# Kernel optimization log

Hardware: AMD Instinct MI355X
Metric: run time of the kernel (lower is better)

Reference implementation:

```python
import jax, jax.numpy as jnp
import numpy as np

BIG = 10000.0

def setup_inputs() -> dict:
    key = jax.random.key(0)
    k1, k2, k3 = jax.random.split(key, 3)
    B, S, D = 32, 4096, 512
    x = jax.random.normal(k1, (B, S, D), dtype=jnp.float32)
    mask = jax.random.randint(k2, (B, S), 0, 2).astype(bool)
    w_attn = jax.random.normal(k3, (D, 1), dtype=jnp.float32)
    return {"x": x, "mask": mask, "w_attn": w_attn}

def reference(x, mask, w_attn):
    # x: [B, S, D], mask: [B, S] bool, w_attn: [D, 1]
    mask_f = mask.astype(jnp.float32)[:, :, None]          # [B, S, 1]
    masked_x = x * mask_f
    seq_len = jnp.sum(mask_f, axis=1) + 1e-6               # [B, 1]
    mean_pool = jnp.sum(masked_x, axis=1) / seq_len        # [B, D]

    m3 = mask[:, :, None]
    max_pool = jnp.max(jnp.where(m3, x, -BIG), axis=1)     # [B, D]
    min_pool = jnp.min(jnp.where(m3, x, BIG), axis=1)      # [B, D]

    attn_scores = jnp.einsum('bsd,do->bso', x, w_attn)     # [B, S, 1]
    attn_scores = jnp.where(m3, attn_scores, -BIG)
    attn_w = jax.nn.softmax(attn_scores, axis=1)           # [B, S, 1]
    attn_pool = jnp.sum(x * attn_w, axis=1)                # [B, D]

    return jnp.concatenate([mean_pool, max_pool, min_pool, attn_pool], axis=-1)
```

## Files before the change

### kernel.cpp

```cpp
#include <hip/hip_runtime.h>
#include <math.h>

#define BIGV 10000.0f

constexpr int B = 32, S = 4096, D = 512;
constexpr int C = 16;
constexpr int L = S / C;
constexpr int T = 16;
constexpr int NT = L / T;
constexpr int BC = B * C;

__global__ __launch_bounds__(512, 4)
void pool_partial(const float* __restrict__ x, const int* __restrict__ mask,
                  const float* __restrict__ w, float* __restrict__ ws) {
  __shared__ float xt[T][D];
  __shared__ float w_s[D];
  __shared__ float sc[T];
  __shared__ float pv[T];
  __shared__ int   mk[T];

  const int tid = threadIdx.x;
  const int blk = blockIdx.x;
  const int b = blk / C, c = blk % C;
  const int s0 = c * L;

  w_s[tid] = w[tid];

  float m = -INFINITY, l = 0.f, cnt = 0.f;
  float o = 0.f, sm = 0.f, mx = -BIGV, mn = BIGV;

  const float4* gsrc = (const float4*)(x + ((size_t)b * S + s0) * D);
  const int* gm = mask + (size_t)b * S + s0;

  const int wave = tid >> 6, lane = tid & 63;

  for (int t = 0; t < NT; ++t) {
    __syncthreads();
    const float4* src = gsrc + (size_t)t * (T * D / 4);
    float4* dst = (float4*)&xt[0][0];
    #pragma unroll
    for (int i = 0; i < (T * D / 4) / 512; ++i)
      dst[tid + i * 512] = src[tid + i * 512];
    if (tid < T) mk[tid] = gm[t * T + tid];
    __syncthreads();

    #pragma unroll
    for (int rr = 0; rr < T / 8; ++rr) {
      const int r = wave * (T / 8) + rr;
      float dacc = 0.f;
      #pragma unroll
      for (int k = 0; k < D / 64; ++k)
        dacc = fmaf(xt[r][lane + 64 * k], w_s[lane + 64 * k], dacc);
      #pragma unroll
      for (int off = 32; off; off >>= 1)
        dacc += __shfl_xor(dacc, off, 64);
      if (lane == 0) sc[r] = mk[r] ? dacc : -BIGV;
    }
    __syncthreads();

    float Mt = -INFINITY;
    #pragma unroll
    for (int r = 0; r < T; ++r) Mt = fmaxf(Mt, sc[r]);
    const float m_new = fmaxf(m, Mt);
    const float alpha = __expf(m - m_new);
    o *= alpha; l *= alpha;
    m = m_new;
    if (tid < T) pv[tid] = __expf(sc[tid] - m_new);
    __syncthreads();

    #pragma unroll
    for (int r = 0; r < T; ++r) {
      const float p    = pv[r];
      const int   mb   = mk[r];
      const float mskf = (float)mb;
      const float xv   = xt[r][tid];
      o  = fmaf(p, xv, o);
      l += p;
      sm = fmaf(mskf, xv, sm);
      mx = fmaxf(mx, mb ? xv : -BIGV);
      mn = fminf(mn, mb ? xv :  BIGV);
      cnt += mskf;
    }
  }

  const size_t idx = (size_t)(b * C + c);
  ws[idx * D + tid]                          = o;
  ws[(size_t)BC * D + idx * D + tid]         = sm;
  ws[2 * (size_t)BC * D + idx * D + tid]     = mx;
  ws[3 * (size_t)BC * D + idx * D + tid]     = mn;
  if (tid == 0) {
    float* scal = ws + 4 * (size_t)BC * D;
    scal[idx]          = m;
    scal[BC + idx]     = l;
    scal[2 * BC + idx] = cnt;
  }
}

__global__ __launch_bounds__(512)
void pool_merge(const float* __restrict__ ws, float* __restrict__ out) {
  const int b = blockIdx.x, tid = threadIdx.x;
  const float* scal = ws + 4 * (size_t)BC * D;

  float m_f = -INFINITY;
  #pragma unroll
  for (int c = 0; c < C; ++c) m_f = fmaxf(m_f, scal[b * C + c]);

  float Lsum = 0.f, CNT = 0.f;
  float o = 0.f, sm = 0.f, mx = -BIGV, mn = BIGV;
  #pragma unroll
  for (int c = 0; c < C; ++c) {
    const size_t idx = (size_t)(b * C + c);
    const float a = __expf(scal[idx] - m_f);
    Lsum += scal[BC + idx] * a;
    CNT  += scal[2 * BC + idx];
    o  = fmaf(ws[idx * D + tid], a, o);
    sm += ws[(size_t)BC * D + idx * D + tid];
    mx  = fmaxf(mx, ws[2 * (size_t)BC * D + idx * D + tid]);
    mn  = fminf(mn, ws[3 * (size_t)BC * D + idx * D + tid]);
  }
  float* ob = out + (size_t)b * 4 * D;
  ob[tid]         = sm / (CNT + 1e-6f);
  ob[D + tid]     = mx;
  ob[2 * D + tid] = mn;
  ob[3 * D + tid] = o / Lsum;
}

extern "C" void kernel_launch(void* const* d_in, const int* in_sizes, int n_in,
                              void* d_out, int out_size, void* d_ws, size_t ws_size,
                              hipStream_t stream) {
  const float* x    = (const float*)d_in[0];
  const int*   mask = (const int*)d_in[1];
  const float* w    = (const float*)d_in[2];
  float* out = (float*)d_out;
  float* ws  = (float*)d_ws;

  pool_partial<<<dim3(B * C), dim3(512), 0, stream>>>(x, mask, w, ws);
  pool_merge<<<dim3(B), dim3(512), 0, stream>>>(ws, out);
}
```

Before: 367.0 us.

## Stream rows per wavefront in registers instead of shared-memory tiles

Replaces the block-wide shared-memory tiling with a design where each 64-lane wave streams its own contiguous row range. Each lane holds 8 columns in registers, prefetches the next row, computes the attention score via shuffle reduction, and updates the online softmax per row. This removes the __syncthreads barriers and LDS traffic, and splits the sequence over more chunks (C=32, 4 waves per block) for more parallel records. In exchange it adds a per-row serial shuffle reduction and exp, plus a larger workspace and merge over 128 records per batch.

```diff
diff --git a/kernel.cpp b/kernel.cpp
--- a/kernel.cpp
+++ b/kernel.cpp
@@ -4,119 +4,117 @@
 #define BIGV 10000.0f
 
 constexpr int B = 32, S = 4096, D = 512;
-constexpr int C = 16;
-constexpr int L = S / C;
-constexpr int T = 16;
-constexpr int NT = L / T;
-constexpr int BC = B * C;
+constexpr int C   = 32;
+constexpr int L   = S / C;
+constexpr int WPB = 4;
+constexpr int RW  = L / WPB;
+constexpr int NREC = B * C * WPB;
+constexpr int RPB  = C * WPB;
 
-__global__ __launch_bounds__(512, 4)
-void pool_partial(const float* __restrict__ x, const int* __restrict__ mask,
-                  const float* __restrict__ w, float* __restrict__ ws) {
-  __shared__ float xt[T][D];
-  __shared__ float w_s[D];
-  __shared__ float sc[T];
-  __shared__ float pv[T];
-  __shared__ int   mk[T];
+__global__ __launch_bounds__(256, 4)
+void pool_stream(const float* __restrict__ x, const int* __restrict__ mask,
+                 const float* __restrict__ wvec, float* __restrict__ ws) {
+  const int tid = threadIdx.x, lane = tid & 63, w = tid >> 6;
+  const int blk = blockIdx.x, b = blk / C, c = blk % C;
+  const int s0 = c * L + w * RW;
 
-  const int tid = threadIdx.x;
-  const int blk = blockIdx.x;
-  const int b = blk / C, c = blk % C;
-  const int s0 = c * L;
+  const float4* xrow4 = (const float4*)(x + ((size_t)b * S + s0) * D);
+  const int*    mr    = mask + (size_t)b * S + s0;
 
-  w_s[tid] = w[tid];
+  const float4* wv4 = (const float4*)wvec;
+  const float4  w0 = wv4[lane * 2], w1 = wv4[lane * 2 + 1];
 
   float m = -INFINITY, l = 0.f, cnt = 0.f;
-  float o = 0.f, sm = 0.f, mx = -BIGV, mn = BIGV;
+  float o[8], sm[8], mx[8], mn[8];
+  #pragma unroll
+  for (int j = 0; j < 8; ++j) { o[j] = 0.f; sm[j] = 0.f; mx[j] = -BIGV; mn[j] = BIGV; }
 
-  const float4* gsrc = (const float4*)(x + ((size_t)b * S + s0) * D);
-  const int* gm = mask + (size_t)b * S + s0;
+  float4 a0 = xrow4[lane * 2];
+  float4 a1 = xrow4[lane * 2 + 1];
+  int    mb = mr[0];
 
-  const int wave = tid >> 6, lane = tid & 63;
+  for (int r = 0; r < RW; ++r) {
+    const float4 c0 = a0, c1 = a1; const int cm = mb;
+    if (r + 1 < RW) {
+      a0 = xrow4[(size_t)(r + 1) * (D / 4) + lane * 2];
+      a1 = xrow4[(size_t)(r + 1) * (D / 4) + lane * 2 + 1];
+      mb = mr[r + 1];
+    }
+    float d = 0.f;
+    d = fmaf(c0.x, w0.x, d); d = fmaf(c0.y, w0.y, d);
+    d = fmaf(c0.z, w0.z, d); d = fmaf(c0.w, w0.w, d);
+    d = fmaf(c1.x, w1.x, d); d = fmaf(c1.y, w1.y, d);
+    d = fmaf(c1.z, w1.z, d); d = fmaf(c1.w, w1.w, d);
+    #pragma unroll
+    for (int off = 32; off; off >>= 1) d += __shfl_xor(d, off, 64);
 
-  for (int t = 0; t < NT; ++t) {
-    __syncthreads();
-    const float4* src = gsrc + (size_t)t * (T * D / 4);
-    float4* dst = (float4*)&xt[0][0];
+    const float s = cm ? d : -BIGV;
+    const float m_new = fmaxf(m, s);
+    if (m_new > m) {
+      const float alpha = __expf(m - m_new);
+      l *= alpha;
+      #pragma unroll
+      for (int j = 0; j < 8; ++j) o[j] *= alpha;
+      m = m_new;
+    }
+    const float p = __expf(s - m);
+    l += p;
+    const float mskf = cm ? 1.f : 0.f;
+    cnt += mskf;
+
+    const float xa[8] = {c0.x, c0.y, c0.z, c0.w, c1.x, c1.y, c1.z, c1.w};
     #pragma unroll
-    for (int i = 0; i < (T * D / 4) / 512; ++i)
-      dst[tid + i * 512] = src[tid + i * 512];
-    if (tid < T) mk[tid] = gm[t * T + tid];
-    __syncthreads();
-
-    #pragma unroll
-    for (int rr = 0; rr < T / 8; ++rr) {
-      const int r = wave * (T / 8) + rr;
-      float dacc = 0.f;
-      #pragma unroll
-      for (int k = 0; k < D / 64; ++k)
-        dacc = fmaf(xt[r][lane + 64 * k], w_s[lane + 64 * k], dacc);
-      #pragma unroll
-      for (int off = 32; off; off >>= 1)
-        dacc += __shfl_xor(dacc, off, 64);
-      if (lane == 0) sc[r] = mk[r] ? dacc : -BIGV;
-    }
-    __syncthreads();
-
-    float Mt = -INFINITY;
-    #pragma unroll
-    for (int r = 0; r < T; ++r) Mt = fmaxf(Mt, sc[r]);
-    const float m_new = fmaxf(m, Mt);
-    const float alpha = __expf(m - m_new);
-    o *= alpha; l *= alpha;
-    m = m_new;
-    if (tid < T) pv[tid] = __expf(sc[tid] - m_new);
-    __syncthreads();
-
-    #pragma unroll
-    for (int r = 0; r < T; ++r) {
-      const float p    = pv[r];
-      const int   mb   = mk[r];
-      const float mskf = (float)mb;
-      const float xv   = xt[r][tid];
-      o  = fmaf(p, xv, o);
-      l += p;
-      sm = fmaf(mskf, xv, sm);
-      mx = fmaxf(mx, mb ? xv : -BIGV);
-      mn = fminf(mn, mb ? xv :  BIGV);
-      cnt += mskf;
+    for (int j = 0; j < 8; ++j) {
+      o[j]  = fmaf(p, xa[j], o[j]);
+      sm[j] = fmaf(mskf, xa[j], sm[j]);
+      mx[j] = fmaxf(mx[j], cm ? xa[j] : -BIGV);
+      mn[j] = fminf(mn[j], cm ? xa[j] :  BIGV);
     }
   }
 
-  const size_t idx = (size_t)(b * C + c);
-  ws[idx * D + tid]                          = o;
-  ws[(size_t)BC * D + idx * D + tid]         = sm;
-  ws[2 * (size_t)BC * D + idx * D + tid]     = mx;
-  ws[3 * (size_t)BC * D + idx * D + tid]     = mn;
-  if (tid == 0) {
-    float* scal = ws + 4 * (size_t)BC * D;
-    scal[idx]          = m;
-    scal[BC + idx]     = l;
-    scal[2 * BC + idx] = cnt;
+  const size_t rec = (size_t)blk * WPB + w;
+  float4* po = (float4*)(ws + rec * D);
+  float4* ps = (float4*)(ws + (size_t)NREC * D + rec * D);
+  float4* px = (float4*)(ws + 2 * (size_t)NREC * D + rec * D);
+  float4* pn = (float4*)(ws + 3 * (size_t)NREC * D + rec * D);
+  po[lane * 2]     = make_float4(o[0], o[1], o[2], o[3]);
+  po[lane * 2 + 1] = make_float4(o[4], o[5], o[6], o[7]);
+  ps[lane * 2]     = make_float4(sm[0], sm[1], sm[2], sm[3]);
+  ps[lane * 2 + 1] = make_float4(sm[4], sm[5], sm[6], sm[7]);
+  px[lane * 2]     = make_float4(mx[0], mx[1], mx[2], mx[3]);
+  px[lane * 2 + 1] = make_float4(mx[4], mx[5], mx[6], mx[7]);
+  pn[lane * 2]     = make_float4(mn[0], mn[1], mn[2], mn[3]);
+  pn[lane * 2 + 1] = make_float4(mn[4], mn[5], mn[6], mn[7]);
+  if (lane == 0) {
+    float* scal = ws + 4 * (size_t)NREC * D;
+    scal[rec]            = m;
+    scal[NREC + rec]     = l;
+    scal[2 * NREC + rec] = cnt;
   }
 }
 
 __global__ __launch_bounds__(512)
 void pool_merge(const float* __restrict__ ws, float* __restrict__ out) {
   const int b = blockIdx.x, tid = threadIdx.x;
-  const float* scal = ws + 4 * (size_t)BC * D;
+  const float* scal = ws + 4 * (size_t)NREC * D;
+  const int r0 = b * RPB;
 
   float m_f = -INFINITY;
-  #pragma unroll
-  for (int c = 0; c < C; ++c) m_f = fmaxf(m_f, scal[b * C + c]);
+  #pragma unroll 4
+  for (int i = 0; i < RPB; ++i) m_f = fmaxf(m_f, scal[r0 + i]);
 
   float Lsum = 0.f, CNT = 0.f;
   float o = 0.f, sm = 0.f, mx = -BIGV, mn = BIGV;
-  #pragma unroll
-  for (int c = 0; c < C; ++c) {
-    const size_t idx = (size_t)(b * C + c);
-    const float a = __expf(scal[idx] - m_f);
-    Lsum += scal[BC + idx] * a;
-    CNT  += scal[2 * BC + idx];
-    o  = fmaf(ws[idx * D + tid], a, o);
-    sm += ws[(size_t)BC * D + idx * D + tid];
-    mx  = fmaxf(mx, ws[2 * (size_t)BC * D + idx * D + tid]);
-    mn  = fminf(mn, ws[3 * (size_t)BC * D + idx * D + tid]);
+  #pragma unroll 4
+  for (int i = 0; i < RPB; ++i) {
+    const size_t rec = (size_t)(r0 + i);
+    const float a = __expf(scal[rec] - m_f);
+    Lsum += scal[NREC + rec] * a;
+    CNT  += scal[2 * NREC + rec];
+    o  = fmaf(ws[rec * D + tid], a, o);
+    sm += ws[(size_t)NREC * D + rec * D + tid];
+    mx  = fmaxf(mx, ws[2 * (size_t)NREC * D + rec * D + tid]);
+    mn  = fminf(mn, ws[3 * (size_t)NREC * D + rec * D + tid]);
   }
   float* ob = out + (size_t)b * 4 * D;
   ob[tid]         = sm / (CNT + 1e-6f);
@@ -134,6 +132,6 @@
   float* out = (float*)d_out;
   float* ws  = (float*)d_ws;
 
-  pool_partial<<<dim3(B * C), dim3(512), 0, stream>>>(x, mask, w, ws);
+  pool_stream<<<dim3(B * C), dim3(256), 0, stream>>>(x, mask, w, ws);
   pool_merge<<<dim3(B), dim3(512), 0, stream>>>(ws, out);
 }
```

Result: slower. 389.4 us (+6.1%).
